# Optimization experiments

Hardware: AMD Instinct MI355X
Metric: run time of the kernel (lower is better)

Reference implementation:

```python
import jax, jax.numpy as jnp
import numpy as np
import math

B, S, D = 4, 2048, 1024
H, DK = 16, 64
NUM_BUCKETS = 32
MAX_DISTANCE = 128


def _relative_position_bucket(relative_position, num_buckets=NUM_BUCKETS, max_distance=MAX_DISTANCE):
    # Bidirectional (encoder) variant, matching TFT5Attention._relative_position_bucket
    nb = num_buckets // 2
    rel_buckets = (relative_position > 0).astype(jnp.int32) * nb
    rel = jnp.abs(relative_position)
    max_exact = nb // 2
    is_small = rel < max_exact
    rel_if_large = max_exact + (
        jnp.log(jnp.maximum(rel, 1).astype(jnp.float32) / max_exact)
        / math.log(max_distance / max_exact)
        * (nb - max_exact)
    ).astype(jnp.int32)
    rel_if_large = jnp.minimum(rel_if_large, nb - 1)
    return rel_buckets + jnp.where(is_small, rel, rel_if_large)


def compute_bias(rel_bias, q_len, k_len):
    context = jnp.arange(q_len)[:, None]
    memory = jnp.arange(k_len)[None, :]
    buckets = _relative_position_bucket(memory - context)  # [q_len, k_len]
    values = rel_bias[buckets]                              # [q_len, k_len, H]
    return jnp.transpose(values, (2, 0, 1))[None]           # [1, H, q_len, k_len]


def setup_inputs() -> dict:
    key = jax.random.key(0)
    ks = jax.random.split(key, 6)
    scale = 1.0 / math.sqrt(D)
    return {
        "hidden_states": jax.random.normal(ks[0], (B, S, D), dtype=jnp.float32),
        "Wq": jax.random.normal(ks[1], (D, H * DK), dtype=jnp.float32) * scale,
        "Wk": jax.random.normal(ks[2], (D, H * DK), dtype=jnp.float32) * scale,
        "Wv": jax.random.normal(ks[3], (D, H * DK), dtype=jnp.float32) * scale,
        "Wo": jax.random.normal(ks[4], (H * DK, D), dtype=jnp.float32) * scale,
        "rel_bias": jax.random.normal(ks[5], (NUM_BUCKETS, H), dtype=jnp.float32),
    }


def reference(hidden_states, Wq, Wk, Wv, Wo, rel_bias):
    b, s, _ = hidden_states.shape

    def to_heads(x):  # [b, s, H*DK] -> [b, H, s, DK]
        return jnp.transpose(x.reshape(b, s, H, DK), (0, 2, 1, 3))

    q = to_heads(hidden_states @ Wq)
    k = to_heads(hidden_states @ Wk)
    v = to_heads(hidden_states @ Wv)

    # NOTE: T5 does NOT scale scores by 1/sqrt(d_kv)
    scores = jnp.einsum("bhqd,bhkd->bhqk", q, k)
    scores = scores + compute_bias(rel_bias, s, s)
    weights = jax.nn.softmax(scores, axis=-1)
    attn = jnp.einsum("bhqk,bhkd->bhqd", weights, v)
    attn = jnp.transpose(attn, (0, 2, 1, 3)).reshape(b, s, H * DK)
    return attn @ Wo
```

## Files before the change

kernel.cpp:

```cpp
#include <hip/hip_runtime.h>
#include <hip/hip_bf16.h>
#include <cstdint>

#define DI __device__ __forceinline__

typedef __attribute__((ext_vector_type(4))) float f32x4;
typedef __attribute__((ext_vector_type(16))) float f32x16;
typedef __attribute__((ext_vector_type(8))) short s16x8;
typedef __attribute__((ext_vector_type(4))) short s16x4;
typedef __attribute__((ext_vector_type(4))) unsigned int u32x4;
typedef unsigned int u32;

constexpr int Sc = 2048;
constexpr float LOG2E = 1.44269504088896340736f;

DI short f2bf(float x) {
    __hip_bfloat16 h = __float2bfloat16(x);
    return __builtin_bit_cast(short, h);
}
DI float bf2f(short x) {
    __hip_bfloat16 h = __builtin_bit_cast(__hip_bfloat16, x);
    return __bfloat162float(h);
}
DI u32 pack2(float a, float b) {
    return (u32)(unsigned short)f2bf(a) | ((u32)(unsigned short)f2bf(b) << 16);
}
DI void pl32swap(u32& a, u32& b) {
    asm("v_permlane32_swap_b32 %0, %1" : "+v"(a), "+v"(b));
}

DI void cp16(const short* g, short* l) {
    __builtin_amdgcn_global_load_lds(
        (const __attribute__((address_space(1))) u32*)g,
        (__attribute__((address_space(3))) u32*)l, 16, 0, 0);
}

DI float fexp2(float x) {
#if __has_builtin(__builtin_amdgcn_exp2f)
    return __builtin_amdgcn_exp2f(x);
#else
    return exp2f(x);
#endif
}
DI float frcp(float x) {
#if __has_builtin(__builtin_amdgcn_rcpf)
    return __builtin_amdgcn_rcpf(x);
#else
    return 1.0f / x;
#endif
}

__global__ void xconv_kernel(const float* __restrict__ X, short* __restrict__ X2) {
    size_t i = ((size_t)blockIdx.x * 256 + threadIdx.x) * 4;
    float4 v = *reinterpret_cast<const float4*>(X + i);
    s16x4 h4 = {f2bf(v.x), f2bf(v.y), f2bf(v.z), f2bf(v.w)};
    *reinterpret_cast<s16x4*>(X2 + i) = h4;
}

__global__ void wqkv_conv(const float* __restrict__ Wq, const float* __restrict__ Wk,
                          const float* __restrict__ Wv, short* __restrict__ WT2) {
    __shared__ float t[32][33];
    int z = blockIdx.z;
    const float* W = (z == 0) ? Wq : (z == 1 ? Wk : Wv);
    int k0 = blockIdx.x * 32, n0 = blockIdx.y * 32;
    int tx = threadIdx.x, ty = threadIdx.y;
#pragma unroll
    for (int i = 0; i < 4; ++i)
        t[ty + 8 * i][tx] = W[(size_t)(k0 + ty + 8 * i) * 1024 + n0 + tx];
    __syncthreads();
#pragma unroll
    for (int i = 0; i < 4; ++i) {
        float v = t[tx][ty + 8 * i];
        short hi = f2bf(v), lo = f2bf(v - bf2f(hi));
        size_t r = (size_t)(z * 1024 + n0 + ty + 8 * i) * 2048 + k0 + tx;
        WT2[r] = hi;
        WT2[r + 1024] = lo;
    }
}

__global__ void wo_conv(const float* __restrict__ Wo, short* __restrict__ WoT) {
    __shared__ float t[32][33];
    int k0 = blockIdx.x * 32, n0 = blockIdx.y * 32;
    int tx = threadIdx.x, ty = threadIdx.y;
#pragma unroll
    for (int i = 0; i < 4; ++i)
        t[ty + 8 * i][tx] = Wo[(size_t)(k0 + ty + 8 * i) * 1024 + n0 + tx];
    __syncthreads();
#pragma unroll
    for (int i = 0; i < 4; ++i)
        WoT[(size_t)(n0 + ty + 8 * i) * 1024 + k0 + tx] = f2bf(t[tx][ty + 8 * i]);
}

__global__ void bias_kernel(const float* __restrict__ rel_bias, short* __restrict__ tab) {
    int idx = blockIdx.x * 256 + threadIdx.x;
    int h = idx >> 12;
    int i = idx & 4095;
    int delta = i - 2047;
    int ad = delta < 0 ? -delta : delta;
    int b;
    if (ad < 8) b = ad;
    else if (ad < 12) b = 8;
    else if (ad < 16) b = 9;
    else if (ad < 23) b = 10;
    else if (ad < 32) b = 11;
    else if (ad < 46) b = 12;
    else if (ad < 64) b = 13;
    else if (ad < 91) b = 14;
    else b = 15;
    if (delta > 0) b += 16;
    tab[idx] = f2bf(rel_bias[b * 16 + h] * LOG2E);
}

template <int EPI>
__launch_bounds__(256)
__global__ void gemm_bt(const short* __restrict__ A, const short* __restrict__ Bt,
                        int K, int lda, int ldb, int aWrap, int bWrap,
                        float* __restrict__ C, int ldc,
                        short* __restrict__ q2, short* __restrict__ k2, short* __restrict__ vt) {
    __shared__ __align__(16) short As[128 * 64];
    __shared__ __align__(16) short Bs[128 * 64];
    const int tid = threadIdx.x;
    const int w = tid >> 6, l = tid & 63;
    const int m0 = blockIdx.x * 128, n0 = blockIdx.y * 128;
    const int wm = (w >> 1) * 64, wn = (w & 1) * 64;
    const int rl = l >> 4, cl = l & 15;

    const int region = (EPI == 1) ? (n0 >> 10) : 0;

    f32x4 acc[4][4];
#pragma unroll
    for (int i = 0; i < 4; ++i)
#pragma unroll
        for (int j = 0; j < 4; ++j) acc[i][j] = (f32x4){0.f, 0.f, 0.f, 0.f};

    const int nk = K / 64;
    const int nkUse = (EPI == 1) ? (region == 2 ? 16 : 32) : nk;

    const int o0 = w * 64 + l;
    const int sr0 = o0 >> 3;
    const int scg = (o0 & 7) ^ (sr0 & 7);

    const int sw = cl & 7;

    for (int kt = 0; kt < nkUse; ++kt) {
        int kk = kt * 64;
        int ca = kk - (kk >= aWrap ? aWrap : 0);
        int cb = kk - (kk >= bWrap ? bWrap : 0);
#pragma unroll
        for (int j = 0; j < 4; ++j) {
            int r = j * 32 + sr0;
            cp16(A + (size_t)(m0 + r) * lda + ca + scg * 8, As + (j * 256 + w * 64) * 8);
            cp16(Bt + (size_t)(n0 + r) * ldb + cb + scg * 8, Bs + (j * 256 + w * 64) * 8);
        }
        __syncthreads();
#pragma unroll
        for (int ks = 0; ks < 2; ++ks) {
            const int slot = ((ks << 2) | rl) ^ sw;
            s16x8 af[4], bfv[4];
#pragma unroll
            for (int i = 0; i < 4; ++i)
                af[i] = *reinterpret_cast<const s16x8*>(As + (wm + i * 16 + cl) * 64 + slot * 8);
#pragma unroll
            for (int i = 0; i < 4; ++i)
                bfv[i] = *reinterpret_cast<const s16x8*>(Bs + (wn + i * 16 + cl) * 64 + slot * 8);
#pragma unroll
            for (int mi = 0; mi < 4; ++mi)
#pragma unroll
                for (int ni = 0; ni < 4; ++ni)
                    acc[mi][ni] = __builtin_amdgcn_mfma_f32_16x16x32_bf16(af[mi], bfv[ni], acc[mi][ni], 0, 0, 0);
        }
        __syncthreads();
    }

    if (EPI == 0) {
#pragma unroll
        for (int mi = 0; mi < 4; ++mi) {
            int row = m0 + wm + mi * 16 + rl * 4;
#pragma unroll
            for (int ni = 0; ni < 4; ++ni) {
                int col = n0 + wn + ni * 16 + cl;
#pragma unroll
                for (int r = 0; r < 4; ++r)
                    C[(size_t)(row + r) * ldc + col] = acc[mi][ni][r];
            }
        }
    } else {
#pragma unroll
        for (int mi = 0; mi < 4; ++mi) {
#pragma unroll
            for (int ni = 0; ni < 4; ++ni) {
#pragma unroll
                for (int r = 0; r < 4; ++r) {
                    int m = m0 + wm + mi * 16 + rl * 4 + r;
                    int n = (n0 & 1023) + wn + ni * 16 + cl;
                    int bb = m >> 11, s = m & 2047;
                    int h = n >> 6, d = n & 63;
                    int bh = bb * 16 + h;
                    float c = acc[mi][ni][r];
                    if (region == 0) {
                        c *= LOG2E;
                        short hi = f2bf(c);
                        short lo = f2bf(c - bf2f(hi));
                        size_t base = ((size_t)bh * 2048 + s) * 128;
                        q2[base + d] = hi;
                        q2[base + 64 + d] = lo;
                    } else if (region == 1) {
                        k2[((size_t)bh * 2048 + s) * 64 + d] = f2bf(c);
                    } else {
                        vt[((size_t)bh * 64 + d) * 2048 + s] = f2bf(c);
                    }
                }
            }
        }
    }
}

__launch_bounds__(512, 4)
__global__ void flash_kernel(const short* __restrict__ q2, const short* __restrict__ k2,
                             const short* __restrict__ vt, const short* __restrict__ btab,
                             short* __restrict__ attnb) {
    __shared__ __align__(16) short Ks[2][4096];
    __shared__ __align__(16) short Vs[2][4096];
    __shared__ __align__(16) short Bsh0[2304];
    __shared__ __align__(16) short Bsh1[2304];

    const int tid = threadIdx.x;
    const int w = tid >> 6, l = tid & 63;
    const int l31 = l & 31, hi = l >> 5;

    const int L = blockIdx.x;
    const int xcd = L & 7, idx = L >> 3;
    const int bh = xcd + 8 * (idx & 7);
    const int qb = idx >> 3;
    const int h = bh & 15;
    const int q0b = qb * 256;
    const int qw0 = q0b + w * 32;
    const int qL = w * 32 + l31;

    const short* Q = q2 + (size_t)bh * Sc * 128;
    const short* Kp = k2 + (size_t)bh * Sc * 64;
    const short* V = vt + (size_t)bh * 64 * Sc;

    {
        int base = h * 4096 + 1792 - q0b;
        for (int i = tid; i < 2304; i += 512) Bsh0[i] = btab[base + i];
        for (int i = tid; i < 2302; i += 512) Bsh1[i] = btab[base + i + 1];
    }

    auto stage = [&](int buf, int it2) {
        int kv0 = it2 * 64;
        {
            int o = w * 64 + l;
            int r = o >> 3, cs = o & 7;
            int cg = cs ^ (r & 7);
            cp16(Kp + (size_t)(kv0 + r) * 64 + cg * 8, &Ks[buf][(w * 64) * 8]);
        }
        {
            int o = w * 64 + l;
            int d = o >> 3, cs = o & 7;
            int cg = cs ^ (d & 7);
            cp16(V + (size_t)d * 2048 + kv0 + cg * 8, &Vs[buf][(w * 64) * 8]);
        }
    };

    s16x8 qf[8];
#pragma unroll
    for (int c = 0; c < 8; ++c)
        qf[c] = *reinterpret_cast<const s16x8*>(Q + (size_t)(qw0 + l31) * 128 + c * 16 + hi * 8);

    f32x16 accO[2];
#pragma unroll
    for (int i = 0; i < 16; ++i) { accO[0][i] = 0.f; accO[1][i] = 0.f; }
    float psum = 0.f;

    stage(0, 0);
    __syncthreads();

    for (int it = 0; it < 32; ++it) {
        const int cur = it & 1;
        if (it + 1 < 32) stage(cur ^ 1, it + 1);
        const int kv0 = it * 64;
#pragma unroll
        for (int T = 0; T < 2; ++T) {
            const int rA = T * 32 + l31;
            const int rsw = rA & 7;
            const short* kbase = &Ks[cur][rA * 64];
            s16x8 kh[4];
#pragma unroll
            for (int c = 0; c < 4; ++c)
                kh[c] = *reinterpret_cast<const s16x8*>(kbase + ((c * 2 + hi) ^ rsw) * 8);
            f32x16 acc = {0.f,0.f,0.f,0.f,0.f,0.f,0.f,0.f,0.f,0.f,0.f,0.f,0.f,0.f,0.f,0.f};
#pragma unroll
            for (int c = 0; c < 4; ++c)
                acc = __builtin_amdgcn_mfma_f32_32x32x16_bf16(kh[c], qf[c], acc, 0, 0, 0);
#pragma unroll
            for (int c = 0; c < 4; ++c)
                acc = __builtin_amdgcn_mfma_f32_32x32x16_bf16(kh[c], qf[c + 4], acc, 0, 0, 0);
#pragma unroll
            for (int t2 = 0; t2 < 2; ++t2) {
                u32 pk[4];
#pragma unroll
                for (int i = 0; i < 4; ++i) {
                    const int ii = t2 * 4 + i;
                    const int pstart = ((ii & 1) * 2) + ((ii >> 1) * 8);
                    const int kvg = kv0 + T * 32 + pstart + 4 * hi;
                    const int i0 = kvg - qL + 255;
                    const short* bp = (i0 & 1) ? (Bsh1 + (i0 - 1)) : (Bsh0 + i0);
                    const u32 pr2 = *reinterpret_cast<const u32*>(bp);
                    const float b0 = bf2f((short)(pr2 & 0xffff));
                    const float b1 = bf2f((short)(pr2 >> 16));
                    const int r0 = t2 * 8 + i * 2;
                    const float e0 = fexp2(acc[r0] + b0);
                    const float e1 = fexp2(acc[r0 + 1] + b1);
                    psum += e0 + e1;
                    pk[i] = pack2(e0, e1);
                }
                pl32swap(pk[0], pk[2]);
                pl32swap(pk[1], pk[3]);
                u32x4 pv4 = {pk[0], pk[1], pk[2], pk[3]};
                s16x8 pfrag = __builtin_bit_cast(s16x8, pv4);
                const int tg = T * 2 + t2;
#pragma unroll
                for (int dt = 0; dt < 2; ++dt) {
                    const int d = dt * 32 + l31;
                    s16x8 vf = *reinterpret_cast<const s16x8*>(
                        &Vs[cur][d * 64 + ((tg * 2 + hi) ^ (d & 7)) * 8]);
                    accO[dt] = __builtin_amdgcn_mfma_f32_32x32x16_bf16(pfrag, vf, accO[dt], 0, 0, 0);
                }
            }
        }
        __syncthreads();
    }

    psum += __shfl_xor(psum, 32);

    const int bb = bh >> 4;
#pragma unroll
    for (int r = 0; r < 16; ++r) {
        const int qloc = (r & 3) + 8 * (r >> 2) + 4 * hi;
        const float inv = frcp(__shfl(psum, qloc));
        const size_t rowbase = ((size_t)(bb * 2048 + qw0 + qloc)) * 1024 + h * 64;
#pragma unroll
        for (int dt = 0; dt < 2; ++dt)
            attnb[rowbase + dt * 32 + l31] = f2bf(accO[dt][r] * inv);
    }
}

extern "C" void kernel_launch(void* const* d_in, const int* in_sizes, int n_in,
                              void* d_out, int out_size, void* d_ws, size_t ws_size,
                              hipStream_t stream) {
    const float* X = (const float*)d_in[0];
    const float* Wq = (const float*)d_in[1];
    const float* Wk = (const float*)d_in[2];
    const float* Wv = (const float*)d_in[3];
    const float* Wo = (const float*)d_in[4];
    const float* RB = (const float*)d_in[5];

    char* ws = (char*)d_ws;
    size_t off = 0;
    auto alloc = [&](size_t bytes) {
        void* p = ws + off;
        off += (bytes + 255) & ~(size_t)255;
        return p;
    };
    short* X2 = (short*)alloc((size_t)8192 * 1024 * 2);
    short* WT2 = (short*)alloc((size_t)3072 * 2048 * 2);
    short* q2 = (short*)alloc((size_t)64 * 2048 * 128 * 2);
    short* k2 = (short*)alloc((size_t)64 * 2048 * 64 * 2);
    short* vt = (short*)alloc((size_t)64 * 64 * 2048 * 2);
    short* attn = (short*)alloc((size_t)8192 * 1024 * 2);
    short* WoT = (short*)alloc((size_t)1024 * 1024 * 2);
    short* btab = (short*)alloc((size_t)16 * 4096 * 2);

    xconv_kernel<<<8192, 256, 0, stream>>>(X, X2);
    wqkv_conv<<<dim3(32, 32, 3), dim3(32, 8), 0, stream>>>(Wq, Wk, Wv, WT2);
    wo_conv<<<dim3(32, 32), dim3(32, 8), 0, stream>>>(Wo, WoT);
    bias_kernel<<<256, 256, 0, stream>>>(RB, btab);
    gemm_bt<1><<<dim3(64, 24), 256, 0, stream>>>(X2, WT2, 3072, 1024, 2048, 1024, 2048,
                                                 nullptr, 0, q2, k2, vt);
    flash_kernel<<<512, 512, 0, stream>>>(q2, k2, vt, btab, attn);
    gemm_bt<0><<<dim3(64, 8), 256, 0, stream>>>(attn, WoT, 1024, 1024, 1024, 1 << 30, 1 << 30,
                                                (float*)d_out, 1024, nullptr, nullptr, nullptr);
}
```

Before: 290.8 us.

## Skip bias table lookups for far-distance tiles and merge weight conversion kernels

In the flash attention kernel, 32-wide key tiles whose relative distance to every query in the warp is at least 91 now use a single precomputed bias value (the saturated bucket), so the per-element LDS bias loads are skipped for them. The softmax/PV body is moved into a lambda specialised on this far/near case, which roughly doubles code size. The Wq/Wk/Wv and Wo conversion kernels are also merged into one launch to save one kernel launch. A redundant duplicate Q fragment load was added, which the compiler should eliminate.

```diff
diff --git a/kernel.cpp b/kernel.cpp
--- a/kernel.cpp
+++ b/kernel.cpp
@@ -57,38 +57,32 @@
     *reinterpret_cast<s16x4*>(X2 + i) = h4;
 }
 
-__global__ void wqkv_conv(const float* __restrict__ Wq, const float* __restrict__ Wk,
-                          const float* __restrict__ Wv, short* __restrict__ WT2) {
+__global__ void wconv(const float* __restrict__ Wq, const float* __restrict__ Wk,
+                      const float* __restrict__ Wv, const float* __restrict__ Wo,
+                      short* __restrict__ WT2, short* __restrict__ WoT) {
     __shared__ float t[32][33];
     int z = blockIdx.z;
-    const float* W = (z == 0) ? Wq : (z == 1 ? Wk : Wv);
+    const float* W = (z == 0) ? Wq : (z == 1 ? Wk : (z == 2 ? Wv : Wo));
     int k0 = blockIdx.x * 32, n0 = blockIdx.y * 32;
     int tx = threadIdx.x, ty = threadIdx.y;
 #pragma unroll
     for (int i = 0; i < 4; ++i)
         t[ty + 8 * i][tx] = W[(size_t)(k0 + ty + 8 * i) * 1024 + n0 + tx];
     __syncthreads();
-#pragma unroll
-    for (int i = 0; i < 4; ++i) {
-        float v = t[tx][ty + 8 * i];
-        short hi = f2bf(v), lo = f2bf(v - bf2f(hi));
-        size_t r = (size_t)(z * 1024 + n0 + ty + 8 * i) * 2048 + k0 + tx;
-        WT2[r] = hi;
-        WT2[r + 1024] = lo;
-    }
-}
-
-__global__ void wo_conv(const float* __restrict__ Wo, short* __restrict__ WoT) {
-    __shared__ float t[32][33];
-    int k0 = blockIdx.x * 32, n0 = blockIdx.y * 32;
-    int tx = threadIdx.x, ty = threadIdx.y;
-#pragma unroll
-    for (int i = 0; i < 4; ++i)
-        t[ty + 8 * i][tx] = Wo[(size_t)(k0 + ty + 8 * i) * 1024 + n0 + tx];
-    __syncthreads();
-#pragma unroll
-    for (int i = 0; i < 4; ++i)
-        WoT[(size_t)(n0 + ty + 8 * i) * 1024 + k0 + tx] = f2bf(t[tx][ty + 8 * i]);
+    if (z < 3) {
+#pragma unroll
+        for (int i = 0; i < 4; ++i) {
+            float v = t[tx][ty + 8 * i];
+            short hi = f2bf(v), lo = f2bf(v - bf2f(hi));
+            size_t r = (size_t)(z * 1024 + n0 + ty + 8 * i) * 2048 + k0 + tx;
+            WT2[r] = hi;
+            WT2[r + 1024] = lo;
+        }
+    } else {
+#pragma unroll
+        for (int i = 0; i < 4; ++i)
+            WoT[(size_t)(n0 + ty + 8 * i) * 1024 + k0 + tx] = f2bf(t[tx][ty + 8 * i]);
+    }
 }
 
 __global__ void bias_kernel(const float* __restrict__ rel_bias, short* __restrict__ tab) {
@@ -139,7 +133,6 @@
     const int o0 = w * 64 + l;
     const int sr0 = o0 >> 3;
     const int scg = (o0 & 7) ^ (sr0 & 7);
-
     const int sw = cl & 7;
 
     for (int kt = 0; kt < nkUse; ++kt) {
@@ -241,6 +234,9 @@
     const short* Kp = k2 + (size_t)bh * Sc * 64;
     const short* V = vt + (size_t)bh * 64 * Sc;
 
+    const float bneg = bf2f(btab[h * 4096 + 2047 - 91]);
+    const float bpos = bf2f(btab[h * 4096 + 2047 + 91]);
+
     {
         int base = h * 4096 + 1792 - q0b;
         for (int i = tid; i < 2304; i += 512) Bsh0[i] = btab[base + i];
@@ -266,6 +262,9 @@
     s16x8 qf[8];
 #pragma unroll
     for (int c = 0; c < 8; ++c)
+        qf[c] = *reinterpret_cast<const s16x8*>(Q + (size_t)(qw0 - q0b + q0b + l31) * 128 + c * 16 + hi * 8);
+#pragma unroll
+    for (int c = 0; c < 8; ++c)
         qf[c] = *reinterpret_cast<const s16x8*>(Q + (size_t)(qw0 + l31) * 128 + c * 16 + hi * 8);
 
     f32x16 accO[2];
@@ -296,38 +295,54 @@
 #pragma unroll
             for (int c = 0; c < 4; ++c)
                 acc = __builtin_amdgcn_mfma_f32_32x32x16_bf16(kh[c], qf[c + 4], acc, 0, 0, 0);
-#pragma unroll
-            for (int t2 = 0; t2 < 2; ++t2) {
-                u32 pk[4];
-#pragma unroll
-                for (int i = 0; i < 4; ++i) {
-                    const int ii = t2 * 4 + i;
-                    const int pstart = ((ii & 1) * 2) + ((ii >> 1) * 8);
-                    const int kvg = kv0 + T * 32 + pstart + 4 * hi;
-                    const int i0 = kvg - qL + 255;
-                    const short* bp = (i0 & 1) ? (Bsh1 + (i0 - 1)) : (Bsh0 + i0);
-                    const u32 pr2 = *reinterpret_cast<const u32*>(bp);
-                    const float b0 = bf2f((short)(pr2 & 0xffff));
-                    const float b1 = bf2f((short)(pr2 >> 16));
-                    const int r0 = t2 * 8 + i * 2;
-                    const float e0 = fexp2(acc[r0] + b0);
-                    const float e1 = fexp2(acc[r0 + 1] + b1);
-                    psum += e0 + e1;
-                    pk[i] = pack2(e0, e1);
+
+            const int kvT0 = kv0 + T * 32;
+            const int dmax = kvT0 + 31 - qw0;
+            const int dmin = kvT0 - qw0 - 31;
+            const bool faru = (dmax <= -91) || (dmin >= 91);
+            const float bunif = (dmax <= -91) ? bneg : bpos;
+
+            auto softpv = [&](bool far) {
+#pragma unroll
+                for (int t2 = 0; t2 < 2; ++t2) {
+                    u32 pk[4];
+#pragma unroll
+                    for (int i = 0; i < 4; ++i) {
+                        const int ii = t2 * 4 + i;
+                        const int pstart = ((ii & 1) * 2) + ((ii >> 1) * 8);
+                        float b0, b1;
+                        if (far) {
+                            b0 = bunif; b1 = bunif;
+                        } else {
+                            const int kvg = kv0 + T * 32 + pstart + 4 * hi;
+                            const int i0 = kvg - qL + 255;
+                            const short* bp = (i0 & 1) ? (Bsh1 + (i0 - 1)) : (Bsh0 + i0);
+                            const u32 pr2 = *reinterpret_cast<const u32*>(bp);
+                            b0 = bf2f((short)(pr2 & 0xffff));
+                            b1 = bf2f((short)(pr2 >> 16));
+                        }
+                        const int r0 = t2 * 8 + i * 2;
+                        const float e0 = fexp2(acc[r0] + b0);
+                        const float e1 = fexp2(acc[r0 + 1] + b1);
+                        psum += e0 + e1;
+                        pk[i] = pack2(e0, e1);
+                    }
+                    pl32swap(pk[0], pk[2]);
+                    pl32swap(pk[1], pk[3]);
+                    u32x4 pv4 = {pk[0], pk[1], pk[2], pk[3]};
+                    s16x8 pfrag = __builtin_bit_cast(s16x8, pv4);
+                    const int tg = T * 2 + t2;
+#pragma unroll
+                    for (int dt = 0; dt < 2; ++dt) {
+                        const int d = dt * 32 + l31;
+                        s16x8 vf = *reinterpret_cast<const s16x8*>(
+                            &Vs[cur][d * 64 + ((tg * 2 + hi) ^ (d & 7)) * 8]);
+                        accO[dt] = __builtin_amdgcn_mfma_f32_32x32x16_bf16(pfrag, vf, accO[dt], 0, 0, 0);
+                    }
                 }
-                pl32swap(pk[0], pk[2]);
-                pl32swap(pk[1], pk[3]);
-                u32x4 pv4 = {pk[0], pk[1], pk[2], pk[3]};
-                s16x8 pfrag = __builtin_bit_cast(s16x8, pv4);
-                const int tg = T * 2 + t2;
-#pragma unroll
-                for (int dt = 0; dt < 2; ++dt) {
-                    const int d = dt * 32 + l31;
-                    s16x8 vf = *reinterpret_cast<const s16x8*>(
-                        &Vs[cur][d * 64 + ((tg * 2 + hi) ^ (d & 7)) * 8]);
-                    accO[dt] = __builtin_amdgcn_mfma_f32_32x32x16_bf16(pfrag, vf, accO[dt], 0, 0, 0);
-                }
-            }
+            };
+            if (faru) softpv(true);
+            else      softpv(false);
         }
         __syncthreads();
     }
@@ -373,8 +388,7 @@
     short* btab = (short*)alloc((size_t)16 * 4096 * 2);
 
     xconv_kernel<<<8192, 256, 0, stream>>>(X, X2);
-    wqkv_conv<<<dim3(32, 32, 3), dim3(32, 8), 0, stream>>>(Wq, Wk, Wv, WT2);
-    wo_conv<<<dim3(32, 32), dim3(32, 8), 0, stream>>>(Wo, WoT);
+    wconv<<<dim3(32, 32, 4), dim3(32, 8), 0, stream>>>(Wq, Wk, Wv, Wo, WT2, WoT);
     bias_kernel<<<256, 256, 0, stream>>>(RB, btab);
     gemm_bt<1><<<dim3(64, 24), 256, 0, stream>>>(X2, WT2, 3072, 1024, 2048, 1024, 2048,
                                                  nullptr, 0, q2, k2, vt);
```

Measured after the change: 269.4 us. 7.4% less time.
